# Kernel tuning notes

Hardware: AMD Instinct MI355X
Metric: run time of the kernel (lower is better)

Reference implementation:

```python
import jax, jax.numpy as jnp
import numpy as np

NUM_NODES = 100000
NUM_REL_P1 = 238  # num_relations + 1 (extra column for self-connection relation id -1)
B = 32768
S = 16
D_IN = 256
D_OUT = 256


def setup_inputs() -> dict:
    key = jax.random.key(0)
    k1, k2, k3, k4, k5 = jax.random.split(key, 5)
    neighbors = jax.random.randint(k1, (B, S), 0, NUM_NODES)          # sampled neighbor node ids
    relations = jax.random.randint(k2, (B, S), 0, NUM_REL_P1)          # sampled relation ids
    features = jax.random.normal(k3, (NUM_NODES, D_IN), dtype=jnp.float32)
    weight = jax.random.normal(k4, (D_OUT, D_IN), dtype=jnp.float32) * (1.0 / np.sqrt(D_IN))
    relation_weight = jax.random.normal(k5, (D_OUT, NUM_REL_P1), dtype=jnp.float32) * 0.05
    return {"neighbors": neighbors, "relations": relations, "features": features,
            "weight": weight, "relation_weight": relation_weight}


def reference(neighbors, relations, features, weight, relation_weight):
    # gather sampled neighbor embeddings: [B, S, D_in]
    neighbor_emb = features[neighbors]
    # mean-aggregate over the sample dim: [B, D_in]
    agg_neighbors = neighbor_emb.mean(axis=1)
    # linear transform: [B, D_in] @ [D_in, D_out] -> [B, D_out]
    agg_neighbors = agg_neighbors @ weight.T
    # gather + mean relation embeddings: [B, S, D_out] -> [B, D_out]
    agg_relations = relation_weight.T[relations].mean(axis=1)
    return jax.nn.relu(agg_neighbors + agg_relations)
```

## Files before the change

### kernel.cpp

```cpp
#include <hip/hip_runtime.h>

#define B_ROWS  32768
#define S_SAMP  16
#define NRELS   238
#define DIM     256
#define N_NODES 100000
#define NF4     ((N_NODES * DIM) / 4)
#define CONV_BLOCKS (NF4 / 256)

typedef __attribute__((ext_vector_type(8))) short  short8;
typedef __attribute__((ext_vector_type(8))) unsigned short ushort8;
typedef __attribute__((ext_vector_type(4))) float  f32x4;

static __device__ __forceinline__ unsigned short f2bf(float f) {
    unsigned int u = __float_as_uint(f);
    u += 0x7FFFu + ((u >> 16) & 1u);
    return (unsigned short)(u >> 16);
}
static __device__ __forceinline__ float bf2f(unsigned short u) {
    return __uint_as_float(((unsigned int)u) << 16);
}

__global__ __launch_bounds__(256) void prep_kernel(const float* __restrict__ F,
                                                   const float* __restrict__ W,
                                                   const float* __restrict__ RW,
                                                   unsigned short* __restrict__ Fb,
                                                   unsigned short* __restrict__ Wb,
                                                   unsigned short* __restrict__ RWTb) {
    if (blockIdx.x < CONV_BLOCKS) {
        int i = blockIdx.x * 256 + threadIdx.x;
        float4 v = ((const float4*)F)[i];
        ushort4 p;
        p.x = f2bf(v.x); p.y = f2bf(v.y); p.z = f2bf(v.z); p.w = f2bf(v.w);
        ((ushort4*)Fb)[i] = p;
    } else {
        int i = (blockIdx.x - CONV_BLOCKS) * 256 + threadIdx.x;
        if (i < DIM * DIM) Wb[i] = f2bf(W[i]);
        if (i < NRELS * DIM) {
            int r = i >> 8;
            int d = i & 255;
            RWTb[i] = f2bf(RW[d * NRELS + r]);
        }
    }
}

__global__ __launch_bounds__(256, 4) void fused_kernel(const int* __restrict__ nbr,
                                                       const int* __restrict__ rels,
                                                       const unsigned short* __restrict__ Fb,
                                                       const unsigned short* __restrict__ RWTb,
                                                       const unsigned short* __restrict__ Wb,
                                                       float* __restrict__ out) {
    __shared__ unsigned short As[32][264];
    __shared__ unsigned short Rs[32][264];
    const int tid  = threadIdx.x;
    const int lane = tid & 63;
    const int wid  = __builtin_amdgcn_readfirstlane(tid >> 6);
    const int half = lane >> 5;
    const int li   = lane & 31;
    const int col0 = lane & 15;
    const int quad = lane >> 4;
    const int r0g  = blockIdx.x * 32;

    const float sc = 1.0f / 16.0f;
    for (int i = 0; i < 8; ++i) {
        const int row_l = wid * 8 + i;
        const int row_g = r0g + row_l;
        const int2* nb2 = (const int2*)(nbr  + row_g * S_SAMP);
        const int2* rl2 = (const int2*)(rels + row_g * S_SAMP);
        float af[8] = {0.f, 0.f, 0.f, 0.f, 0.f, 0.f, 0.f, 0.f};
        float ag[8] = {0.f, 0.f, 0.f, 0.f, 0.f, 0.f, 0.f, 0.f};
#pragma unroll
        for (int t = 0; t < 8; ++t) {
            int2 nn = nb2[t];
            int2 rr = rl2[t];
            int nid = half ? nn.y : nn.x;
            int rid = half ? rr.y : rr.x;
            ushort8 f = *(const ushort8*)(Fb   + (size_t)nid * DIM + li * 8);
            ushort8 g = *(const ushort8*)(RWTb + (size_t)rid * DIM + li * 8);
#pragma unroll
            for (int j = 0; j < 8; ++j) { af[j] += bf2f(f[j]); ag[j] += bf2f(g[j]); }
        }
        ushort8 pk;
#pragma unroll
        for (int j = 0; j < 8; ++j) {
            float mine = half ? ag[j] : af[j];
            float send = half ? af[j] : ag[j];
            float full = mine + __shfl_xor(send, 32, 64);
            pk[j] = f2bf(full * sc);
        }
        unsigned short* dst = half ? &Rs[row_l][li * 8] : &As[row_l][li * 8];
        *(ushort8*)dst = pk;
    }

    short8 Breg[4][4];
#pragma unroll
    for (int j = 0; j < 4; ++j)
#pragma unroll
        for (int kk = 0; kk < 4; ++kk)
            Breg[j][kk] = *(const short8*)(Wb + (size_t)((wid * 4 + j) * 16 + col0) * DIM
                                              + kk * 32 + quad * 8);
    __syncthreads();

    f32x4 acc[2][4];
#pragma unroll
    for (int mt = 0; mt < 2; ++mt)
#pragma unroll
        for (int j = 0; j < 4; ++j) acc[mt][j] = (f32x4){0.f, 0.f, 0.f, 0.f};

#pragma unroll
    for (int mt = 0; mt < 2; ++mt) {
        const int mrow = mt * 16 + col0;
#pragma unroll
        for (int kk = 0; kk < 4; ++kk) {
            short8 a = *(const short8*)&As[mrow][kk * 32 + quad * 8];
#pragma unroll
            for (int j = 0; j < 4; ++j)
                acc[mt][j] = __builtin_amdgcn_mfma_f32_16x16x32_bf16(a, Breg[j][kk], acc[mt][j], 0, 0, 0);
        }
    }
#pragma unroll
    for (int j = 0; j < 4; ++j)
#pragma unroll
        for (int kk = 0; kk < 4; ++kk)
            Breg[j][kk] = *(const short8*)(Wb + (size_t)((wid * 4 + j) * 16 + col0) * DIM
                                              + (kk + 4) * 32 + quad * 8);
#pragma unroll
    for (int mt = 0; mt < 2; ++mt) {
        const int mrow = mt * 16 + col0;
#pragma unroll
        for (int kk = 0; kk < 4; ++kk) {
            short8 a = *(const short8*)&As[mrow][(kk + 4) * 32 + quad * 8];
#pragma unroll
            for (int j = 0; j < 4; ++j)
                acc[mt][j] = __builtin_amdgcn_mfma_f32_16x16x32_bf16(a, Breg[j][kk], acc[mt][j], 0, 0, 0);
        }
    }

#pragma unroll
    for (int mt = 0; mt < 2; ++mt) {
#pragma unroll
        for (int j = 0; j < 4; ++j) {
            const int col = (wid * 4 + j) * 16 + col0;
#pragma unroll
            for (int i2 = 0; i2 < 4; ++i2) {
                const int r_l = mt * 16 + quad * 4 + i2;
                float v = acc[mt][j][i2] + bf2f(Rs[r_l][col]);
                out[(size_t)(r0g + r_l) * DIM + col] = v > 0.f ? v : 0.f;
            }
        }
    }
}

extern "C" void kernel_launch(void* const* d_in, const int* in_sizes, int n_in,
                              void* d_out, int out_size, void* d_ws, size_t ws_size,
                              hipStream_t stream) {
    const int*   neighbors = (const int*)d_in[0];
    const int*   relations = (const int*)d_in[1];
    const float* features  = (const float*)d_in[2];
    const float* weight    = (const float*)d_in[3];
    const float* relw      = (const float*)d_in[4];
    float* out = (float*)d_out;

    char* ws = (char*)d_ws;
    unsigned short* Wb   = (unsigned short*)ws;
    unsigned short* RWTb = (unsigned short*)(ws + 131072);
    unsigned short* Fb   = (unsigned short*)(ws + 253952);

    prep_kernel<<<CONV_BLOCKS + 256, 256, 0, stream>>>(features, weight, relw, Fb, Wb, RWTb);
    fused_kernel<<<B_ROWS / 32, 256, 0, stream>>>(neighbors, relations, Fb, RWTb, Wb, out);
}
```

Before: 219.0 us.

## Replace relation-embedding gather with histogram counts times relation weight via MFMA

Instead of gathering 16 relation-weight rows per output row and averaging, each block builds a per-row histogram of relation ids with packed 4-bit counters in shared memory (LDS atomics). The histograms are converted to bf16 count/16 and multiplied against the bf16 relation-weight matrix with MFMA, accumulating into the same accumulator as the feature GEMM. This removes half of the gather traffic and the shuffle merge, but adds LDS atomics, an extra barrier and a second K=256 GEMM per block. The packed 4-bit counters only hold 0 to 15, so a row where all 16 samples share one relation id would overflow its nibble.

New measurement: 225.8 us. 1.03x slower.

```diff
diff --git a/kernel.cpp b/kernel.cpp
--- a/kernel.cpp
+++ b/kernel.cpp
@@ -26,7 +26,7 @@
                                                    const float* __restrict__ RW,
                                                    unsigned short* __restrict__ Fb,
                                                    unsigned short* __restrict__ Wb,
-                                                   unsigned short* __restrict__ RWTb) {
+                                                   unsigned short* __restrict__ RWb) {
     if (blockIdx.x < CONV_BLOCKS) {
         int i = blockIdx.x * 256 + threadIdx.x;
         float4 v = ((const float4*)F)[i];
@@ -35,11 +35,11 @@
         ((ushort4*)Fb)[i] = p;
     } else {
         int i = (blockIdx.x - CONV_BLOCKS) * 256 + threadIdx.x;
-        if (i < DIM * DIM) Wb[i] = f2bf(W[i]);
-        if (i < NRELS * DIM) {
-            int r = i >> 8;
-            int d = i & 255;
-            RWTb[i] = f2bf(RW[d * NRELS + r]);
+        if (i < DIM * DIM) {
+            Wb[i] = f2bf(W[i]);
+            int n = i >> 8;
+            int k = i & 255;
+            RWb[i] = (k < NRELS) ? f2bf(RW[n * NRELS + k]) : (unsigned short)0;
         }
     }
 }
@@ -47,11 +47,12 @@
 __global__ __launch_bounds__(256, 4) void fused_kernel(const int* __restrict__ nbr,
                                                        const int* __restrict__ rels,
                                                        const unsigned short* __restrict__ Fb,
-                                                       const unsigned short* __restrict__ RWTb,
+                                                       const unsigned short* __restrict__ RWb,
                                                        const unsigned short* __restrict__ Wb,
                                                        float* __restrict__ out) {
     __shared__ unsigned short As[32][264];
-    __shared__ unsigned short Rs[32][264];
+    __shared__ unsigned short Cs[32][264];
+    __shared__ unsigned int   cnt4[32][32];
     const int tid  = threadIdx.x;
     const int lane = tid & 63;
     const int wid  = __builtin_amdgcn_readfirstlane(tid >> 6);
@@ -61,35 +62,40 @@
     const int quad = lane >> 4;
     const int r0g  = blockIdx.x * 32;
 
+    unsigned int* c4 = (unsigned int*)cnt4;
+    c4[tid] = 0u; c4[tid + 256] = 0u; c4[tid + 512] = 0u; c4[tid + 768] = 0u;
+    __syncthreads();
+
+    {
+        const int hr = tid >> 3;
+        const int hs = tid & 7;
+        int rid0 = rels[(r0g + hr) * S_SAMP + hs];
+        int rid1 = rels[(r0g + hr) * S_SAMP + hs + 8];
+        atomicAdd(&cnt4[hr][rid0 >> 3], 1u << ((rid0 & 7) * 4));
+        atomicAdd(&cnt4[hr][rid1 >> 3], 1u << ((rid1 & 7) * 4));
+    }
+
     const float sc = 1.0f / 16.0f;
     for (int i = 0; i < 8; ++i) {
         const int row_l = wid * 8 + i;
         const int row_g = r0g + row_l;
-        const int2* nb2 = (const int2*)(nbr  + row_g * S_SAMP);
-        const int2* rl2 = (const int2*)(rels + row_g * S_SAMP);
+        const int2* nb2 = (const int2*)(nbr + row_g * S_SAMP);
         float af[8] = {0.f, 0.f, 0.f, 0.f, 0.f, 0.f, 0.f, 0.f};
-        float ag[8] = {0.f, 0.f, 0.f, 0.f, 0.f, 0.f, 0.f, 0.f};
 #pragma unroll
         for (int t = 0; t < 8; ++t) {
             int2 nn = nb2[t];
-            int2 rr = rl2[t];
             int nid = half ? nn.y : nn.x;
-            int rid = half ? rr.y : rr.x;
-            ushort8 f = *(const ushort8*)(Fb   + (size_t)nid * DIM + li * 8);
-            ushort8 g = *(const ushort8*)(RWTb + (size_t)rid * DIM + li * 8);
-#pragma unroll
-            for (int j = 0; j < 8; ++j) { af[j] += bf2f(f[j]); ag[j] += bf2f(g[j]); }
+            ushort8 f = *(const ushort8*)(Fb + (size_t)nid * DIM + li * 8);
+#pragma unroll
+            for (int j = 0; j < 8; ++j) af[j] += bf2f(f[j]);
         }
         ushort8 pk;
 #pragma unroll
         for (int j = 0; j < 8; ++j) {
-            float mine = half ? ag[j] : af[j];
-            float send = half ? af[j] : ag[j];
-            float full = mine + __shfl_xor(send, 32, 64);
+            float full = af[j] + __shfl_xor(af[j], 32, 64);
             pk[j] = f2bf(full * sc);
         }
-        unsigned short* dst = half ? &Rs[row_l][li * 8] : &As[row_l][li * 8];
-        *(ushort8*)dst = pk;
+        if (!half) *(ushort8*)&As[row_l][li * 8] = pk;
     }
 
     short8 Breg[4][4];
@@ -101,6 +107,21 @@
                                               + kk * 32 + quad * 8);
     __syncthreads();
 
+    {
+        const int rr = tid >> 3;
+        const int kb = (tid & 7) * 32;
+#pragma unroll
+        for (int g = 0; g < 4; ++g) {
+            unsigned int w = cnt4[rr][(kb >> 3) + g];
+            ushort8 ck;
+#pragma unroll
+            for (int j = 0; j < 8; ++j)
+                ck[j] = f2bf((float)((w >> (4 * j)) & 0xFu) * 0.0625f);
+            *(ushort8*)&Cs[rr][kb + g * 8] = ck;
+        }
+    }
+    __syncthreads();
+
     f32x4 acc[2][4];
 #pragma unroll
     for (int mt = 0; mt < 2; ++mt)
@@ -135,6 +156,40 @@
                 acc[mt][j] = __builtin_amdgcn_mfma_f32_16x16x32_bf16(a, Breg[j][kk], acc[mt][j], 0, 0, 0);
         }
     }
+#pragma unroll
+    for (int j = 0; j < 4; ++j)
+#pragma unroll
+        for (int kk = 0; kk < 4; ++kk)
+            Breg[j][kk] = *(const short8*)(RWb + (size_t)((wid * 4 + j) * 16 + col0) * DIM
+                                               + kk * 32 + quad * 8);
+#pragma unroll
+    for (int mt = 0; mt < 2; ++mt) {
+        const int mrow = mt * 16 + col0;
+#pragma unroll
+        for (int kk = 0; kk < 4; ++kk) {
+            short8 a = *(const short8*)&Cs[mrow][kk * 32 + quad * 8];
+#pragma unroll
+            for (int j = 0; j < 4; ++j)
+                acc[mt][j] = __builtin_amdgcn_mfma_f32_16x16x32_bf16(a, Breg[j][kk], acc[mt][j], 0, 0, 0);
+        }
+    }
+#pragma unroll
+    for (int j = 0; j < 4; ++j)
+#pragma unroll
+        for (int kk = 0; kk < 4; ++kk)
+            Breg[j][kk] = *(const short8*)(RWb + (size_t)((wid * 4 + j) * 16 + col0) * DIM
+                                               + (kk + 4) * 32 + quad * 8);
+#pragma unroll
+    for (int mt = 0; mt < 2; ++mt) {
+        const int mrow = mt * 16 + col0;
+#pragma unroll
+        for (int kk = 0; kk < 4; ++kk) {
+            short8 a = *(const short8*)&Cs[mrow][(kk + 4) * 32 + quad * 8];
+#pragma unroll
+            for (int j = 0; j < 4; ++j)
+                acc[mt][j] = __builtin_amdgcn_mfma_f32_16x16x32_bf16(a, Breg[j][kk], acc[mt][j], 0, 0, 0);
+        }
+    }
 
 #pragma unroll
     for (int mt = 0; mt < 2; ++mt) {
@@ -144,7 +199,7 @@
 #pragma unroll
             for (int i2 = 0; i2 < 4; ++i2) {
                 const int r_l = mt * 16 + quad * 4 + i2;
-                float v = acc[mt][j][i2] + bf2f(Rs[r_l][col]);
+                float v = acc[mt][j][i2];
                 out[(size_t)(r0g + r_l) * DIM + col] = v > 0.f ? v : 0.f;
             }
         }
@@ -162,10 +217,10 @@
     float* out = (float*)d_out;
 
     char* ws = (char*)d_ws;
-    unsigned short* Wb   = (unsigned short*)ws;
-    unsigned short* RWTb = (unsigned short*)(ws + 131072);
-    unsigned short* Fb   = (unsigned short*)(ws + 253952);
-
-    prep_kernel<<<CONV_BLOCKS + 256, 256, 0, stream>>>(features, weight, relw, Fb, Wb, RWTb);
-    fused_kernel<<<B_ROWS / 32, 256, 0, stream>>>(neighbors, relations, Fb, RWTb, Wb, out);
-}
+    unsigned short* Wb  = (unsigned short*)ws;
+    unsigned short* RWb = (unsigned short*)(ws + 131072);
+    unsigned short* Fb  = (unsigned short*)(ws + 262144);
+
+    prep_kernel<<<CONV_BLOCKS + 256, 256, 0, stream>>>(features, weight, relw, Fb, Wb, RWb);
+    fused_kernel<<<B_ROWS / 32, 256, 0, stream>>>(neighbors, relations, Fb, RWb, Wb, out);
+}
```
